# Optimization experiments

Hardware: AMD Instinct MI355X
Metric: run time of the kernel (lower is better)

Reference implementation:

```python
import jax, jax.numpy as jnp
import numpy as np

N_EXPERTS = 64
TOP_K = 2
LOAD_BALANCE_COEF = 0.01
D_MODEL = 4096
N_TOKENS = 16384


def setup_inputs() -> dict:
    key = jax.random.key(0)
    kx, kw = jax.random.split(key)
    x = jax.random.normal(kx, (N_TOKENS, D_MODEL), dtype=jnp.float32)
    # nn.init.normal_(gate.weight, std=0.01); shape (n_experts, d_model)
    gate_w = 0.01 * jax.random.normal(kw, (N_EXPERTS, D_MODEL), dtype=jnp.float32)
    return {"x": x, "gate_w": gate_w}


def reference(x, gate_w):
    # logits: (N, n_experts)
    logits = jnp.einsum('nd,ed->ne', x, gate_w)
    router_probs = jax.nn.softmax(logits, axis=-1)
    top_k_weights, top_k_indices = jax.lax.top_k(router_probs, TOP_K)
    routing_weights = top_k_weights / jnp.sum(top_k_weights, axis=-1, keepdims=True)
    top1 = top_k_indices[:, 0]
    one_hot = jax.nn.one_hot(top1, N_EXPERTS, dtype=x.dtype)  # (N, n_experts)
    f_i = jnp.mean(one_hot, axis=0)          # fraction of tokens per expert (detached)
    p_i = jnp.mean(router_probs, axis=0)     # mean router prob per expert (diff.)
    load_balance_loss = LOAD_BALANCE_COEF * jnp.sum(jax.lax.stop_gradient(f_i) * p_i)
    return routing_weights, top_k_indices, load_balance_loss
```

## Files before the change

### kernel.cpp

```cpp
#include <hip/hip_runtime.h>
#include <math.h>

#define N_TOKENS 16384
#define D_MODEL  4096
#define N_EXP    64

#define BK   16
#define LD   68
#define NW   8
#define KW   (D_MODEL / NW)
#define NT   (KW / BK)
#define NBLK (N_TOKENS / 64)

__global__ void __launch_bounds__(256)
transpose_w(const float* __restrict__ w, float* __restrict__ wt) {
    __shared__ float t[64][LD];
    const int k0 = blockIdx.x * 64;
    const int kc = (threadIdx.x & 15) * 4;
    const int e0 = threadIdx.x >> 4;
#pragma unroll
    for (int p = 0; p < 4; ++p) {
        int e = p * 16 + e0;
        float4 v = *(const float4*)(w + (size_t)e * D_MODEL + k0 + kc);
        t[kc + 0][e] = v.x; t[kc + 1][e] = v.y;
        t[kc + 2][e] = v.z; t[kc + 3][e] = v.w;
    }
    __syncthreads();
    const int kr = threadIdx.x >> 2;
    const int ec = (threadIdx.x & 3) * 16;
#pragma unroll
    for (int j = 0; j < 4; ++j) {
        float4 v = make_float4(t[kr][ec + j * 4 + 0], t[kr][ec + j * 4 + 1],
                               t[kr][ec + j * 4 + 2], t[kr][ec + j * 4 + 3]);
        *(float4*)(wt + (size_t)(k0 + kr) * N_EXP + ec + j * 4) = v;
    }
}

__global__ void __launch_bounds__(512, 2)
router_fused(const float* __restrict__ x, const float* __restrict__ wt,
             float* __restrict__ out, float* __restrict__ block_sums) {
    __shared__ float smem[NW * 2 * BK * LD];

    const int tid  = threadIdx.x;
    const int wv   = tid >> 6;
    const int lane = tid & 63;
    const int tok0 = blockIdx.x * 64;

    float* xs = smem + wv * (2 * BK * LD);

    const int srow = lane >> 2;
    const int skc  = (lane & 3) * 4;

    const int trow = (lane & 7) * 8;
    const int ecol = (lane >> 3) * 8;

    const float* xp = x + (size_t)(tok0 + srow) * D_MODEL + (size_t)wv * KW + skc;
    const float* wp = wt + (size_t)wv * KW * N_EXP + ecol;

    float acc[8][8] = {};

#define LOADR(q, roff) (*(const float4*)((q) + (size_t)(roff) * D_MODEL))
#define STORE_TILE(buf, v, roff) do {                      \
        (buf)[(skc + 0) * LD + srow + (roff)] = (v).x;     \
        (buf)[(skc + 1) * LD + srow + (roff)] = (v).y;     \
        (buf)[(skc + 2) * LD + srow + (roff)] = (v).z;     \
        (buf)[(skc + 3) * LD + srow + (roff)] = (v).w;     \
    } while (0)

    {
        float4 a0 = LOADR(xp, 0),  a1 = LOADR(xp, 16);
        float4 a2 = LOADR(xp, 32), a3 = LOADR(xp, 48);
        STORE_TILE(xs, a0, 0);  STORE_TILE(xs, a1, 16);
        STORE_TILE(xs, a2, 32); STORE_TILE(xs, a3, 48);
    }

    auto compute_tile = [&](const float* xb, int kbase) {
#pragma unroll 4
        for (int k = 0; k < BK; ++k) {
            const float* xr = xb + k * LD + trow;
            float4 xa = *(const float4*)xr;
            float4 xc = *(const float4*)(xr + 4);
            const float* wr = wp + (size_t)(kbase + k) * N_EXP;
            float4 wa = *(const float4*)wr;
            float4 wc = *(const float4*)(wr + 4);
            float xf[8] = {xa.x, xa.y, xa.z, xa.w, xc.x, xc.y, xc.z, xc.w};
            float wf[8] = {wa.x, wa.y, wa.z, wa.w, wc.x, wc.y, wc.z, wc.w};
#pragma unroll
            for (int i = 0; i < 8; ++i)
#pragma unroll
                for (int j = 0; j < 8; ++j)
                    acc[i][j] = fmaf(xf[i], wf[j], acc[i][j]);
        }
    };

    for (int t = 0; t < NT - 1; ++t) {
        float* xb = xs + (t & 1) * (BK * LD);
        float* xn = xs + ((t + 1) & 1) * (BK * LD);

        const float* xq = xp + (t + 1) * BK;
        float4 a0 = LOADR(xq, 0),  a1 = LOADR(xq, 16);
        float4 a2 = LOADR(xq, 32), a3 = LOADR(xq, 48);

        compute_tile(xb, t * BK);

        STORE_TILE(xn, a0, 0);  STORE_TILE(xn, a1, 16);
        STORE_TILE(xn, a2, 32); STORE_TILE(xn, a3, 48);
    }
    compute_tile(xs + ((NT - 1) & 1) * (BK * LD), (NT - 1) * BK);

    __syncthreads();

    float* tile = smem + (wv & 3) * 4096;
    if (wv < 4) {
#pragma unroll
        for (int i = 0; i < 8; ++i) {
            *(float4*)&tile[(trow + i) * 64 + ecol] =
                make_float4(acc[i][0], acc[i][1], acc[i][2], acc[i][3]);
            *(float4*)&tile[(trow + i) * 64 + ecol + 4] =
                make_float4(acc[i][4], acc[i][5], acc[i][6], acc[i][7]);
        }
    }
    __syncthreads();
    if (wv >= 4) {
#pragma unroll
        for (int i = 0; i < 8; ++i) {
            float4* tp = (float4*)&tile[(trow + i) * 64 + ecol];
            float4 v0 = tp[0], v1 = tp[1];
            v0.x += acc[i][0]; v0.y += acc[i][1];
            v0.z += acc[i][2]; v0.w += acc[i][3];
            v1.x += acc[i][4]; v1.y += acc[i][5];
            v1.z += acc[i][6]; v1.w += acc[i][7];
            tp[0] = v0; tp[1] = v1;
        }
    }
    __syncthreads();

    float p_acc = 0.f, f_acc = 0.f;
#pragma unroll 1
    for (int it = 0; it < 8; ++it) {
        const int tl = wv * 8 + it;
        const int o  = tl * 64 + lane;
        float logit = smem[o] + smem[4096 + o] + smem[8192 + o] + smem[12288 + o];

        float m = logit;
#pragma unroll
        for (int off = 32; off; off >>= 1)
            m = fmaxf(m, __shfl_xor(m, off, 64));
        unsigned long long b1 = __ballot(logit == m);
        int i1 = __ffsll(b1) - 1;

        float p = expf(logit - m);
        float denom = p;
#pragma unroll
        for (int off = 32; off; off >>= 1)
            denom += __shfl_xor(denom, off, 64);

        p_acc += p / denom;
        if (lane == i1) f_acc += 1.f;

        float lx = (lane == i1) ? -__builtin_inff() : logit;
        float m2 = lx;
#pragma unroll
        for (int off = 32; off; off >>= 1)
            m2 = fmaxf(m2, __shfl_xor(m2, off, 64));
        unsigned long long b2 = __ballot(lx == m2);
        int i2 = __ffsll(b2) - 1;

        if (lane == 0) {
            float p1 = 1.0f / denom;
            float p2 = expf(m2 - m) / denom;
            float s12 = p1 + p2;
            int token = tok0 + tl;
            ((float2*)out)[token] = make_float2(p1 / s12, p2 / s12);
            ((float2*)(out + 2 * N_TOKENS))[token] =
                make_float2((float)i1, (float)i2);
        }
    }

    float* pf = smem + 4 * 4096;
    pf[wv * 64 + lane]       = p_acc;
    pf[512 + wv * 64 + lane] = f_acc;
    __syncthreads();
    if (tid < N_EXP) {
        float ps = 0.f, fs = 0.f;
#pragma unroll
        for (int h = 0; h < NW; ++h) {
            ps += pf[h * 64 + tid];
            fs += pf[512 + h * 64 + tid];
        }
        block_sums[(size_t)blockIdx.x * 128 + tid]      = ps;
        block_sums[(size_t)blockIdx.x * 128 + 64 + tid] = fs;
    }
}

__global__ void __launch_bounds__(256)
router_final(const float* __restrict__ block_sums, float* __restrict__ out) {
    __shared__ float sp[4][N_EXP];
    __shared__ float sf[4][N_EXP];

    int tid  = threadIdx.x;
    int wv   = tid >> 6;
    int lane = tid & 63;

    float ps = 0.f, fs = 0.f;
#pragma unroll 8
    for (int b = wv * (NBLK / 4); b < (wv + 1) * (NBLK / 4); ++b) {
        ps += block_sums[(size_t)b * 128 + lane];
        fs += block_sums[(size_t)b * 128 + 64 + lane];
    }
    sp[wv][lane] = ps;
    sf[wv][lane] = fs;
    __syncthreads();

    if (tid < N_EXP) {
        float pt = sp[0][tid] + sp[1][tid] + sp[2][tid] + sp[3][tid];
        float ft = sf[0][tid] + sf[1][tid] + sf[2][tid] + sf[3][tid];
        float v = pt * ft;
#pragma unroll
        for (int off = 1; off < 64; off <<= 1)
            v += __shfl_xor(v, off, 64);
        if (tid == 0)
            out[4 * N_TOKENS] = 0.01f * v / ((float)N_TOKENS * (float)N_TOKENS);
    }
}

extern "C" void kernel_launch(void* const* d_in, const int* in_sizes, int n_in,
                              void* d_out, int out_size, void* d_ws, size_t ws_size,
                              hipStream_t stream) {
    (void)in_sizes; (void)n_in; (void)out_size; (void)ws_size;
    const float* x = (const float*)d_in[0];
    const float* w = (const float*)d_in[1];
    float* out = (float*)d_out;

    float* wT = (float*)d_ws;
    float* block_sums = wT + (size_t)D_MODEL * N_EXP;

    transpose_w<<<D_MODEL / 64, 256, 0, stream>>>(w, wT);
    router_fused<<<NBLK, 512, 0, stream>>>(x, wT, out, block_sums);
    router_final<<<1, 256, 0, stream>>>(block_sums, out);
}
```

Baseline: 499.7 us.

## Halve token tile and stage weight tiles through LDS per wave

Shrinks the per-block token tile from 64 to 32, doubling the block count, and cuts the per-thread accumulator tile from 8x8 to 4x8. Weight rows are now double-buffered in LDS alongside x instead of being read from global memory inside the inner loop, and BK drops from 16 to 8. The launch-bounds occupancy hint of 2 is removed. The aim is more parallelism and lower register pressure, in exchange for weight traffic per token doubling because each weight row serves fewer tokens.

New measurement: 417.3 us. -16.5%, faster.

```diff
diff --git a/kernel.cpp b/kernel.cpp
--- a/kernel.cpp
+++ b/kernel.cpp
@@ -5,16 +5,19 @@
 #define D_MODEL  4096
 #define N_EXP    64
 
-#define BK   16
-#define LD   68
+#define TOKB 32
 #define NW   8
 #define KW   (D_MODEL / NW)
+#define BK   8
 #define NT   (KW / BK)
-#define NBLK (N_TOKENS / 64)
+#define LDX  36
+#define LDW  68
+#define SZW  (2 * BK * LDX + 2 * BK * LDW)
+#define NBLK (N_TOKENS / TOKB)
 
 __global__ void __launch_bounds__(256)
 transpose_w(const float* __restrict__ w, float* __restrict__ wt) {
-    __shared__ float t[64][LD];
+    __shared__ float t[64][LDW];
     const int k0 = blockIdx.x * 64;
     const int kc = (threadIdx.x & 15) * 4;
     const int e0 = threadIdx.x >> 4;
@@ -36,84 +39,92 @@
     }
 }
 
-__global__ void __launch_bounds__(512, 2)
+__global__ void __launch_bounds__(512)
 router_fused(const float* __restrict__ x, const float* __restrict__ wt,
              float* __restrict__ out, float* __restrict__ block_sums) {
-    __shared__ float smem[NW * 2 * BK * LD];
+    __shared__ float smem[NW * SZW];
 
     const int tid  = threadIdx.x;
     const int wv   = tid >> 6;
     const int lane = tid & 63;
-    const int tok0 = blockIdx.x * 64;
-
-    float* xs = smem + wv * (2 * BK * LD);
-
-    const int srow = lane >> 2;
-    const int skc  = (lane & 3) * 4;
-
-    const int trow = (lane & 7) * 8;
+    const int tok0 = blockIdx.x * TOKB;
+
+    float* xs = smem + wv * SZW;
+    float* wl = xs + 2 * BK * LDX;
+
+    const int srow = lane >> 1;
+    const int skc  = (lane & 1) * 4;
+    const int kk   = lane >> 3;
+    const int ec   = (lane & 7) * 8;
+
+    const int trow = (lane & 7) * 4;
     const int ecol = (lane >> 3) * 8;
 
     const float* xp = x + (size_t)(tok0 + srow) * D_MODEL + (size_t)wv * KW + skc;
-    const float* wp = wt + (size_t)wv * KW * N_EXP + ecol;
-
-    float acc[8][8] = {};
-
-#define LOADR(q, roff) (*(const float4*)((q) + (size_t)(roff) * D_MODEL))
-#define STORE_TILE(buf, v, roff) do {                      \
-        (buf)[(skc + 0) * LD + srow + (roff)] = (v).x;     \
-        (buf)[(skc + 1) * LD + srow + (roff)] = (v).y;     \
-        (buf)[(skc + 2) * LD + srow + (roff)] = (v).z;     \
-        (buf)[(skc + 3) * LD + srow + (roff)] = (v).w;     \
+    const float* wp = wt + ((size_t)wv * KW + kk) * N_EXP + ec;
+
+    float acc[4][8] = {};
+
+#define STORE_X(buf, v) do {                               \
+        (buf)[(skc + 0) * LDX + srow] = (v).x;             \
+        (buf)[(skc + 1) * LDX + srow] = (v).y;             \
+        (buf)[(skc + 2) * LDX + srow] = (v).z;             \
+        (buf)[(skc + 3) * LDX + srow] = (v).w;             \
     } while (0)
+#define STORE_W(buf, u0, u1) do {                          \
+        *(float4*)&(buf)[kk * LDW + ec]     = (u0);        \
+        *(float4*)&(buf)[kk * LDW + ec + 4] = (u1);        \
+    } while (0)
 
     {
-        float4 a0 = LOADR(xp, 0),  a1 = LOADR(xp, 16);
-        float4 a2 = LOADR(xp, 32), a3 = LOADR(xp, 48);
-        STORE_TILE(xs, a0, 0);  STORE_TILE(xs, a1, 16);
-        STORE_TILE(xs, a2, 32); STORE_TILE(xs, a3, 48);
-    }
-
-    auto compute_tile = [&](const float* xb, int kbase) {
-#pragma unroll 4
+        float4 a  = *(const float4*)(xp);
+        float4 b0 = *(const float4*)(wp);
+        float4 b1 = *(const float4*)(wp + 4);
+        STORE_X(xs, a);
+        STORE_W(wl, b0, b1);
+    }
+
+    auto compute_tile = [&](const float* xb, const float* wb) {
+#pragma unroll
         for (int k = 0; k < BK; ++k) {
-            const float* xr = xb + k * LD + trow;
-            float4 xa = *(const float4*)xr;
-            float4 xc = *(const float4*)(xr + 4);
-            const float* wr = wp + (size_t)(kbase + k) * N_EXP;
-            float4 wa = *(const float4*)wr;
-            float4 wc = *(const float4*)(wr + 4);
-            float xf[8] = {xa.x, xa.y, xa.z, xa.w, xc.x, xc.y, xc.z, xc.w};
+            float4 xa = *(const float4*)&xb[k * LDX + trow];
+            float4 wa = *(const float4*)&wb[k * LDW + ecol];
+            float4 wc = *(const float4*)&wb[k * LDW + ecol + 4];
+            float xf[4] = {xa.x, xa.y, xa.z, xa.w};
             float wf[8] = {wa.x, wa.y, wa.z, wa.w, wc.x, wc.y, wc.z, wc.w};
 #pragma unroll
-            for (int i = 0; i < 8; ++i)
+            for (int i = 0; i < 4; ++i)
 #pragma unroll
                 for (int j = 0; j < 8; ++j)
                     acc[i][j] = fmaf(xf[i], wf[j], acc[i][j]);
         }
     };
 
+#pragma unroll 2
     for (int t = 0; t < NT - 1; ++t) {
-        float* xb = xs + (t & 1) * (BK * LD);
-        float* xn = xs + ((t + 1) & 1) * (BK * LD);
-
-        const float* xq = xp + (t + 1) * BK;
-        float4 a0 = LOADR(xq, 0),  a1 = LOADR(xq, 16);
-        float4 a2 = LOADR(xq, 32), a3 = LOADR(xq, 48);
-
-        compute_tile(xb, t * BK);
-
-        STORE_TILE(xn, a0, 0);  STORE_TILE(xn, a1, 16);
-        STORE_TILE(xn, a2, 32); STORE_TILE(xn, a3, 48);
-    }
-    compute_tile(xs + ((NT - 1) & 1) * (BK * LD), (NT - 1) * BK);
-
-    __syncthreads();
-
-    float* tile = smem + (wv & 3) * 4096;
+        float* xb = xs + (t & 1) * (BK * LDX);
+        float* wb = wl + (t & 1) * (BK * LDW);
+        float* xn = xs + ((t + 1) & 1) * (BK * LDX);
+        float* wn = wl + ((t + 1) & 1) * (BK * LDW);
+
+        float4 a  = *(const float4*)(xp + (t + 1) * BK);
+        float4 b0 = *(const float4*)(wp + (size_t)(t + 1) * BK * N_EXP);
+        float4 b1 = *(const float4*)(wp + (size_t)(t + 1) * BK * N_EXP + 4);
+
+        compute_tile(xb, wb);
+
+        STORE_X(xn, a);
+        STORE_W(wn, b0, b1);
+    }
+    compute_tile(xs + ((NT - 1) & 1) * (BK * LDX),
+                 wl + ((NT - 1) & 1) * (BK * LDW));
+
+    __syncthreads();
+
+    float* tile = smem + (wv & 3) * (TOKB * N_EXP);
     if (wv < 4) {
 #pragma unroll
-        for (int i = 0; i < 8; ++i) {
+        for (int i = 0; i < 4; ++i) {
             *(float4*)&tile[(trow + i) * 64 + ecol] =
                 make_float4(acc[i][0], acc[i][1], acc[i][2], acc[i][3]);
             *(float4*)&tile[(trow + i) * 64 + ecol + 4] =
@@ -123,7 +134,7 @@
     __syncthreads();
     if (wv >= 4) {
 #pragma unroll
-        for (int i = 0; i < 8; ++i) {
+        for (int i = 0; i < 4; ++i) {
             float4* tp = (float4*)&tile[(trow + i) * 64 + ecol];
             float4 v0 = tp[0], v1 = tp[1];
             v0.x += acc[i][0]; v0.y += acc[i][1];
@@ -137,10 +148,10 @@
 
     float p_acc = 0.f, f_acc = 0.f;
 #pragma unroll 1
-    for (int it = 0; it < 8; ++it) {
-        const int tl = wv * 8 + it;
+    for (int it = 0; it < 4; ++it) {
+        const int tl = wv * 4 + it;
         const int o  = tl * 64 + lane;
-        float logit = smem[o] + smem[4096 + o] + smem[8192 + o] + smem[12288 + o];
+        float logit = smem[o] + smem[2048 + o] + smem[4096 + o] + smem[6144 + o];
 
         float m = logit;
 #pragma unroll
@@ -177,7 +188,7 @@
         }
     }
 
-    float* pf = smem + 4 * 4096;
+    float* pf = smem + 4 * TOKB * N_EXP;
     pf[wv * 64 + lane]       = p_acc;
     pf[512 + wv * 64 + lane] = f_acc;
     __syncthreads();
```
